# Kernel tuning notes

Hardware: AMD Instinct MI355X
Metric: run time of the kernel (lower is better)

## Reference

```python
import jax, jax.numpy as jnp
import numpy as np

B, IN_F, OUT_F, KD = 256, 1024, 128, 16


def setup_inputs() -> dict:
    key = jax.random.key(0)
    k1, k2 = jax.random.split(key)
    x = jax.random.normal(k1, (B, IN_F), dtype=jnp.float32)
    t_mat = jax.random.normal(k2, (IN_F, OUT_F, KD), dtype=jnp.float32)
    return {"x": x, "t_mat": t_mat}


def reference(x, t_mat):
    # Projection: [B, in] @ [in, out*kd] -> [B, out, kd]
    m = jnp.einsum('bi,iok->bok', x, t_mat)
    # All-pairs L1 distance over kernel dim: [B, B, out]
    norm = jnp.sum(jnp.abs(m[:, None, :, :] - m[None, :, :, :]), axis=-1)
    # exp(-norm) summed over the partner axis; subtract 1 for self-pair (norm=0 -> exp=1)
    o_b = jnp.sum(jnp.exp(-norm), axis=1) - 1.0  # [B, out]
    return jnp.concatenate([x, o_b], axis=1)  # [B, in + out]
```

## Files before the change

kernel.cpp:

```cpp
#include <hip/hip_runtime.h>
#include <hip/hip_fp16.h>


#define BATCH 256
#define INF   1024
#define OUTF  128
#define KDIM  16
#define TCOLS 2048
#define OCOLS 1152
#define XB    1032
#define PMW   12

typedef __attribute__((ext_vector_type(8))) short short8;
typedef __attribute__((ext_vector_type(4))) float f32x4;
typedef __attribute__((ext_vector_type(4))) unsigned short ushort4v;

__device__ inline unsigned short bf_trunc(float f) {
    return (unsigned short)(__float_as_uint(f) >> 16);
}

__global__ __launch_bounds__(256) void k_prep(const float* __restrict__ x,
                                              unsigned short* __restrict__ xs,
                                              float* __restrict__ out) {
    const int b = blockIdx.x, t = threadIdx.x;
    const int i = b * 256 + t;
    float4 v = reinterpret_cast<const float4*>(x)[i];
    ushort4v o4 = { bf_trunc(v.x), bf_trunc(v.y), bf_trunc(v.z), bf_trunc(v.w) };
    reinterpret_cast<ushort4v*>(xs)[i] = o4;
    reinterpret_cast<float4*>(out)[b * 288 + t] = v;
}

__global__ __launch_bounds__(1024, 4) void k_fused(const float* __restrict__ T,
                                                   const unsigned short* __restrict__ xs,
                                                   float* __restrict__ out) {
    const int blk = blockIdx.x;
    const int o   = blk & 127;
    const int h   = blk >> 7;
    const int tid = threadIdx.x;
    const int wave = tid >> 6, lane = tid & 63;
    const int l15 = lane & 15, q = lane >> 4;

    __shared__ unsigned short bs[16][XB];
    __shared__ __half2 pm[BATCH][PMW];
    __shared__ float part[32][128];

    {
        const int kb = tid >> 2, n0 = (tid & 3) * 4;
        float4 tv[4];
        #pragma unroll
        for (int pass = 0; pass < 4; ++pass)
            tv[pass] = *reinterpret_cast<const float4*>(
                &T[(pass * 256 + kb) * TCOLS + o * KDIM + n0]);
        #pragma unroll
        for (int pass = 0; pass < 4; ++pass) {
            const int k = pass * 256 + kb;
            bs[n0 + 0][k] = bf_trunc(tv[pass].x);
            bs[n0 + 1][k] = bf_trunc(tv[pass].y);
            bs[n0 + 2][k] = bf_trunc(tv[pass].z);
            bs[n0 + 3][k] = bf_trunc(tv[pass].w);
        }
    }
    __syncthreads();

    const unsigned short* xr = xs + (wave * 16 + l15) * INF + q * 8;

    f32x4 acc = {0.f, 0.f, 0.f, 0.f};
    {
        short8 A[8], Bb[8];
        #pragma unroll
        for (int i = 0; i < 8; ++i) A[i]  = *reinterpret_cast<const short8*>(xr + i * 32);
        #pragma unroll
        for (int i = 0; i < 8; ++i) Bb[i] = *reinterpret_cast<const short8*>(xr + (8 + i) * 32);
        __builtin_amdgcn_sched_barrier(0);

        #pragma unroll
        for (int ks = 0; ks < 8; ++ks) {
            short8 bfr = *reinterpret_cast<const short8*>(&bs[l15][ks * 32 + q * 8]);
            acc = __builtin_amdgcn_mfma_f32_16x16x32_bf16(A[ks], bfr, acc, 0, 0, 0);
        }
        #pragma unroll
        for (int i = 0; i < 8; ++i) A[i] = *reinterpret_cast<const short8*>(xr + (16 + i) * 32);
        #pragma unroll
        for (int ks = 8; ks < 16; ++ks) {
            short8 bfr = *reinterpret_cast<const short8*>(&bs[l15][ks * 32 + q * 8]);
            acc = __builtin_amdgcn_mfma_f32_16x16x32_bf16(Bb[ks - 8], bfr, acc, 0, 0, 0);
        }
        #pragma unroll
        for (int i = 0; i < 8; ++i) Bb[i] = *reinterpret_cast<const short8*>(xr + (24 + i) * 32);
        #pragma unroll
        for (int ks = 16; ks < 24; ++ks) {
            short8 bfr = *reinterpret_cast<const short8*>(&bs[l15][ks * 32 + q * 8]);
            acc = __builtin_amdgcn_mfma_f32_16x16x32_bf16(A[ks - 16], bfr, acc, 0, 0, 0);
        }
        #pragma unroll
        for (int ks = 24; ks < 32; ++ks) {
            short8 bfr = *reinterpret_cast<const short8*>(&bs[l15][ks * 32 + q * 8]);
            acc = __builtin_amdgcn_mfma_f32_16x16x32_bf16(Bb[ks - 24], bfr, acc, 0, 0, 0);
        }
    }

    {
        __half* pmh = reinterpret_cast<__half*>(pm);
        #pragma unroll
        for (int r = 0; r < 4; ++r)
            pmh[(wave * 16 + q * 4 + r) * (2 * PMW) + l15] = __float2half(acc[r]);
    }
    __syncthreads();

    const int i1 = tid & 31;
    const int bsel = tid >> 5;
    __half2 my[4][8];
    #pragma unroll
    for (int r = 0; r < 4; ++r) {
        union { uint4 u[2]; __half2 hh[8]; } c;
        c.u[0] = *reinterpret_cast<const uint4*>(&pm[h * 128 + r * 32 + i1][0]);
        c.u[1] = *reinterpret_cast<const uint4*>(&pm[h * 128 + r * 32 + i1][4]);
        #pragma unroll
        for (int j = 0; j < 8; ++j) my[r][j] = c.hh[j];
    }

    union U16 { uint4 u[2]; __half2 hh[8]; };
    float tot[4] = {0.f, 0.f, 0.f, 0.f};
    const int b2_lo = bsel * 8;

    U16 c0, c1;
    c0.u[0] = *reinterpret_cast<const uint4*>(&pm[b2_lo][0]);
    c0.u[1] = *reinterpret_cast<const uint4*>(&pm[b2_lo][4]);

    #pragma unroll
    for (int ib = 0; ib < 8; ib += 2) {
        c1.u[0] = *reinterpret_cast<const uint4*>(&pm[b2_lo + ib + 1][0]);
        c1.u[1] = *reinterpret_cast<const uint4*>(&pm[b2_lo + ib + 1][4]);
        #pragma unroll
        for (int r = 0; r < 4; ++r) {
            __half2 e0 = __habs2(__hsub2(my[r][0], c0.hh[0]));
            __half2 e1 = __habs2(__hsub2(my[r][1], c0.hh[1]));
            __half2 e2 = __habs2(__hsub2(my[r][2], c0.hh[2]));
            __half2 e3 = __habs2(__hsub2(my[r][3], c0.hh[3]));
            e0 = __hadd2(e0, __habs2(__hsub2(my[r][4], c0.hh[4])));
            e1 = __hadd2(e1, __habs2(__hsub2(my[r][5], c0.hh[5])));
            e2 = __hadd2(e2, __habs2(__hsub2(my[r][6], c0.hh[6])));
            e3 = __hadd2(e3, __habs2(__hsub2(my[r][7], c0.hh[7])));
            __half2 es = __hadd2(__hadd2(e0, e1), __hadd2(e2, e3));
            float n = __low2float(es) + __high2float(es);
            tot[r] += __expf(-n);
        }
        if (ib + 2 < 8) {
            c0.u[0] = *reinterpret_cast<const uint4*>(&pm[b2_lo + ib + 2][0]);
            c0.u[1] = *reinterpret_cast<const uint4*>(&pm[b2_lo + ib + 2][4]);
        }
        #pragma unroll
        for (int r = 0; r < 4; ++r) {
            __half2 e0 = __habs2(__hsub2(my[r][0], c1.hh[0]));
            __half2 e1 = __habs2(__hsub2(my[r][1], c1.hh[1]));
            __half2 e2 = __habs2(__hsub2(my[r][2], c1.hh[2]));
            __half2 e3 = __habs2(__hsub2(my[r][3], c1.hh[3]));
            e0 = __hadd2(e0, __habs2(__hsub2(my[r][4], c1.hh[4])));
            e1 = __hadd2(e1, __habs2(__hsub2(my[r][5], c1.hh[5])));
            e2 = __hadd2(e2, __habs2(__hsub2(my[r][6], c1.hh[6])));
            e3 = __hadd2(e3, __habs2(__hsub2(my[r][7], c1.hh[7])));
            __half2 es = __hadd2(__hadd2(e0, e1), __hadd2(e2, e3));
            float n = __low2float(es) + __high2float(es);
            tot[r] += __expf(-n);
        }
    }
    #pragma unroll
    for (int r = 0; r < 4; ++r)
        part[bsel][r * 32 + i1] = tot[r];
    __syncthreads();

    {
        const int g = tid >> 7, b1 = tid & 127;
        float s = part[g * 4 + 0][b1] + part[g * 4 + 1][b1]
                + part[g * 4 + 2][b1] + part[g * 4 + 3][b1];
        __syncthreads();
        part[g * 4][b1] = s;
    }
    __syncthreads();
    if (tid < 128) {
        float s = -1.0f;
        #pragma unroll
        for (int g = 0; g < 8; ++g) s += part[g * 4][tid];
        out[(h * 128 + tid) * OCOLS + INF + o] = s;
    }
}

extern "C" void kernel_launch(void* const* d_in, const int* in_sizes, int n_in,
                              void* d_out, int out_size, void* d_ws, size_t ws_size,
                              hipStream_t stream) {
    const float* x = (const float*)d_in[0];
    const float* T = (const float*)d_in[1];
    float* out = (float*)d_out;
    unsigned short* xs = (unsigned short*)d_ws;

    k_prep<<<256, 256, 0, stream>>>(x, xs, out);
    k_fused<<<256, 1024, 0, stream>>>(T, xs, out);
}
```

Baseline: 86.74 us.

## Split fused kernel into separate GEMM and pairwise kernels to avoid redundant projection

Measured after the change: 83.06 us. 1.04x faster.

```diff
diff --git a/kernel.cpp b/kernel.cpp
--- a/kernel.cpp
+++ b/kernel.cpp
@@ -30,80 +30,91 @@
     reinterpret_cast<float4*>(out)[b * 288 + t] = v;
 }
 
-__global__ __launch_bounds__(1024, 4) void k_fused(const float* __restrict__ T,
-                                                   const unsigned short* __restrict__ xs,
-                                                   float* __restrict__ out) {
+__global__ __launch_bounds__(256, 2) void k_gemm(const float* __restrict__ T,
+                                                 const unsigned short* __restrict__ xs,
+                                                 __half* __restrict__ mh) {
+    const int blk = blockIdx.x;
+    const int o   = blk & 127;
+    const int mq  = blk >> 7;
+    const int tid = threadIdx.x;
+    const int wave = tid >> 6, lane = tid & 63;
+    const int l15 = lane & 15, q = lane >> 4;
+
+    __shared__ unsigned short bs[16][XB];
+    __shared__ __half pmout[64][16];
+
+    const int mt = mq * 4 + wave;
+    const unsigned short* xr = xs + (mt * 16 + l15) * INF + q * 8;
+
+    short8 a[16];
+    #pragma unroll
+    for (int i = 0; i < 16; ++i)
+        a[i] = *reinterpret_cast<const short8*>(xr + i * 32);
+    __builtin_amdgcn_sched_barrier(0);
+
+    {
+        const int kb = tid >> 2, n0 = (tid & 3) * 4;
+        #pragma unroll
+        for (int g = 0; g < 4; ++g) {
+            float4 tv[4];
+            #pragma unroll
+            for (int p = 0; p < 4; ++p)
+                tv[p] = *reinterpret_cast<const float4*>(
+                    &T[((g * 4 + p) * 64 + kb) * TCOLS + o * KDIM + n0]);
+            #pragma unroll
+            for (int p = 0; p < 4; ++p) {
+                const int k = (g * 4 + p) * 64 + kb;
+                bs[n0 + 0][k] = bf_trunc(tv[p].x);
+                bs[n0 + 1][k] = bf_trunc(tv[p].y);
+                bs[n0 + 2][k] = bf_trunc(tv[p].z);
+                bs[n0 + 3][k] = bf_trunc(tv[p].w);
+            }
+        }
+    }
+    __syncthreads();
+
+    f32x4 acc = {0.f, 0.f, 0.f, 0.f};
+    #pragma unroll
+    for (int ks = 0; ks < 16; ++ks) {
+        short8 bfr = *reinterpret_cast<const short8*>(&bs[l15][ks * 32 + q * 8]);
+        acc = __builtin_amdgcn_mfma_f32_16x16x32_bf16(a[ks], bfr, acc, 0, 0, 0);
+    }
+    #pragma unroll
+    for (int i = 0; i < 16; ++i)
+        a[i] = *reinterpret_cast<const short8*>(xr + (16 + i) * 32);
+    __builtin_amdgcn_sched_barrier(0);
+    #pragma unroll
+    for (int ks = 0; ks < 16; ++ks) {
+        short8 bfr = *reinterpret_cast<const short8*>(&bs[l15][(16 + ks) * 32 + q * 8]);
+        acc = __builtin_amdgcn_mfma_f32_16x16x32_bf16(a[ks], bfr, acc, 0, 0, 0);
+    }
+
+    #pragma unroll
+    for (int r = 0; r < 4; ++r)
+        pmout[wave * 16 + q * 4 + r][l15] = __float2half(acc[r]);
+    __syncthreads();
+
+    if (tid < 128) {
+        const int row = tid >> 1, hh = tid & 1;
+        uint4 v = *reinterpret_cast<const uint4*>(&pmout[row][hh * 8]);
+        *reinterpret_cast<uint4*>(&mh[o * (BATCH * KDIM) + (mq * 64 + row) * KDIM + hh * 8]) = v;
+    }
+}
+
+__global__ __launch_bounds__(1024, 4) void k_pair(const __half* __restrict__ mh,
+                                                  float* __restrict__ out) {
     const int blk = blockIdx.x;
     const int o   = blk & 127;
     const int h   = blk >> 7;
     const int tid = threadIdx.x;
-    const int wave = tid >> 6, lane = tid & 63;
-    const int l15 = lane & 15, q = lane >> 4;
-
-    __shared__ unsigned short bs[16][XB];
+
     __shared__ __half2 pm[BATCH][PMW];
     __shared__ float part[32][128];
 
-    {
-        const int kb = tid >> 2, n0 = (tid & 3) * 4;
-        float4 tv[4];
-        #pragma unroll
-        for (int pass = 0; pass < 4; ++pass)
-            tv[pass] = *reinterpret_cast<const float4*>(
-                &T[(pass * 256 + kb) * TCOLS + o * KDIM + n0]);
-        #pragma unroll
-        for (int pass = 0; pass < 4; ++pass) {
-            const int k = pass * 256 + kb;
-            bs[n0 + 0][k] = bf_trunc(tv[pass].x);
-            bs[n0 + 1][k] = bf_trunc(tv[pass].y);
-            bs[n0 + 2][k] = bf_trunc(tv[pass].z);
-            bs[n0 + 3][k] = bf_trunc(tv[pass].w);
-        }
-    }
-    __syncthreads();
-
-    const unsigned short* xr = xs + (wave * 16 + l15) * INF + q * 8;
-
-    f32x4 acc = {0.f, 0.f, 0.f, 0.f};
-    {
-        short8 A[8], Bb[8];
-        #pragma unroll
-        for (int i = 0; i < 8; ++i) A[i]  = *reinterpret_cast<const short8*>(xr + i * 32);
-        #pragma unroll
-        for (int i = 0; i < 8; ++i) Bb[i] = *reinterpret_cast<const short8*>(xr + (8 + i) * 32);
-        __builtin_amdgcn_sched_barrier(0);
-
-        #pragma unroll
-        for (int ks = 0; ks < 8; ++ks) {
-            short8 bfr = *reinterpret_cast<const short8*>(&bs[l15][ks * 32 + q * 8]);
-            acc = __builtin_amdgcn_mfma_f32_16x16x32_bf16(A[ks], bfr, acc, 0, 0, 0);
-        }
-        #pragma unroll
-        for (int i = 0; i < 8; ++i) A[i] = *reinterpret_cast<const short8*>(xr + (16 + i) * 32);
-        #pragma unroll
-        for (int ks = 8; ks < 16; ++ks) {
-            short8 bfr = *reinterpret_cast<const short8*>(&bs[l15][ks * 32 + q * 8]);
-            acc = __builtin_amdgcn_mfma_f32_16x16x32_bf16(Bb[ks - 8], bfr, acc, 0, 0, 0);
-        }
-        #pragma unroll
-        for (int i = 0; i < 8; ++i) Bb[i] = *reinterpret_cast<const short8*>(xr + (24 + i) * 32);
-        #pragma unroll
-        for (int ks = 16; ks < 24; ++ks) {
-            short8 bfr = *reinterpret_cast<const short8*>(&bs[l15][ks * 32 + q * 8]);
-            acc = __builtin_amdgcn_mfma_f32_16x16x32_bf16(A[ks - 16], bfr, acc, 0, 0, 0);
-        }
-        #pragma unroll
-        for (int ks = 24; ks < 32; ++ks) {
-            short8 bfr = *reinterpret_cast<const short8*>(&bs[l15][ks * 32 + q * 8]);
-            acc = __builtin_amdgcn_mfma_f32_16x16x32_bf16(Bb[ks - 24], bfr, acc, 0, 0, 0);
-        }
-    }
-
-    {
-        __half* pmh = reinterpret_cast<__half*>(pm);
-        #pragma unroll
-        for (int r = 0; r < 4; ++r)
-            pmh[(wave * 16 + q * 4 + r) * (2 * PMW) + l15] = __float2half(acc[r]);
+    if (tid < 512) {
+        uint4 v = *reinterpret_cast<const uint4*>(
+            &mh[o * (BATCH * KDIM) + (tid >> 1) * KDIM + (tid & 1) * 8]);
+        *reinterpret_cast<uint4*>(&pm[tid >> 1][(tid & 1) * 4]) = v;
     }
     __syncthreads();
 
@@ -192,7 +203,9 @@
     const float* T = (const float*)d_in[1];
     float* out = (float*)d_out;
     unsigned short* xs = (unsigned short*)d_ws;
+    __half* mh = (__half*)((char*)d_ws + (1u << 20));
 
     k_prep<<<256, 256, 0, stream>>>(x, xs, out);
-    k_fused<<<256, 1024, 0, stream>>>(T, xs, out);
-}
+    k_gemm<<<512, 256, 0, stream>>>(T, xs, mh);
+    k_pair<<<256, 1024, 0, stream>>>(mh, out);
+}
```
